# Kernel tuning notes

Hardware: AMD Instinct MI355X
Metric: run time of the kernel (lower is better)

Reference implementation:

```python
import jax, jax.numpy as jnp
import numpy as np

B, N_FEAT, SEQ, E, H, V = 32, 196, 64, 1024, 1024, 32000


def setup_inputs() -> dict:
    key = jax.random.key(0)
    ks = jax.random.split(key, 16)
    s = 0.02
    return {
        "features": jax.random.normal(ks[0], (B, N_FEAT, E), jnp.float32),
        "captions": jax.random.randint(ks[1], (B, SEQ), 0, V),
        "max_seq_length": SEQ,
        # decoder embedding table (vocab, embed)
        "emb": jax.random.normal(ks[2], (V, E), jnp.float32) * s,
        # attention MLP: Linear(E->H), Tanh, Linear(H->1)
        "Wa1": jax.random.normal(ks[3], (H, E), jnp.float32) * s,
        "ba1": jnp.zeros((H,), jnp.float32),
        "Wa2": jax.random.normal(ks[4], (1, H), jnp.float32) * s,
        "ba2": jnp.zeros((1,), jnp.float32),
        # GRU (1 layer), input = concat(word_emb, context) -> E + H
        "W_ih": jax.random.normal(ks[5], (3 * H, E + H), jnp.float32) * s,
        "W_hh": jax.random.normal(ks[6], (3 * H, H), jnp.float32) * s,
        "b_ih": jnp.zeros((3 * H,), jnp.float32),
        "b_hh": jnp.zeros((3 * H,), jnp.float32),
        # output projection Linear(H -> V)
        "W_fc": jax.random.normal(ks[7], (V, H), jnp.float32) * s,
        "b_fc": jnp.zeros((V,), jnp.float32),
    }


def reference(features, captions, max_seq_length, emb, Wa1, ba1, Wa2, ba2,
              W_ih, W_hh, b_ih, b_hh, W_fc, b_fc):
    # words: (B, S, E)
    words = emb[captions]
    # combined: (B, N_FEAT + S, E)
    combined = jnp.concatenate([features, words], axis=1)
    # attention scores over the combined tokens, softmax along token axis
    scores = jnp.tanh(combined @ Wa1.T + ba1) @ Wa2.T + ba2   # (B, M, 1)
    A = jax.nn.softmax(scores, axis=1)                         # (B, M, 1)
    # context h0 = A^T @ combined -> (B, E); used both as GRU h0 and per-step context
    h0 = jnp.sum(A * combined, axis=1)
    context = h0

    def gru_cell(x, h):
        gi = x @ W_ih.T + b_ih          # (B, 3H)
        gh = h @ W_hh.T + b_hh          # (B, 3H)
        ir, iz, inn = jnp.split(gi, 3, axis=-1)
        hr, hz, hn = jnp.split(gh, 3, axis=-1)
        r = jax.nn.sigmoid(ir + hr)
        z = jax.nn.sigmoid(iz + hz)
        n = jnp.tanh(inn + r * hn)
        return (1.0 - z) * n + z * h

    def step(carry, _):
        input_word, h = carry
        x = jnp.concatenate([emb[input_word], context], axis=-1)  # (B, E+H)
        h_new = gru_cell(x, h)
        out = h_new @ W_fc.T + b_fc                               # (B, V)
        # greedy feedback (eval path / no teacher forcing)
        next_word = jnp.argmax(out, axis=-1)
        return (next_word, h_new), out

    init = (captions[:, 0], h0)
    (_, _), outs = jax.lax.scan(step, init, None, length=max_seq_length - 1)
    outs = jnp.transpose(outs, (1, 0, 2))                         # (B, S-1, V)
    bsz = captions.shape[0]
    vocab = W_fc.shape[0]
    outputs = jnp.concatenate(
        [jnp.zeros((bsz, 1, vocab), outs.dtype), outs], axis=1)   # t=0 stays zero
    return outputs, A
```

## Files before the change

### kernel.cpp

```cpp
#include <hip/hip_runtime.h>
#include <hip/hip_bf16.h>

typedef unsigned long long ull;
typedef unsigned int uint;

#define NB 32
#define NFEAT 196
#define SEQL 64
#define ED 1024
#define HD 1024
#define VOC 32000
#define NCOMB 260
#define NROWS (NB*NCOMB)
#define NTILE 2000

typedef __attribute__((ext_vector_type(8))) short s16x8;
typedef __attribute__((ext_vector_type(4))) float f32x4;
typedef __attribute__((ext_vector_type(4))) uint  u32x4;

union FragU { u32x4 u; s16x8 s; };

#define DOT4(acc, wv, xv) acc = fmaf((wv).x,(xv).x, fmaf((wv).y,(xv).y, fmaf((wv).z,(xv).z, fmaf((wv).w,(xv).w,(acc)))))

__device__ __forceinline__ uint enc_f32(float f) {
    uint u = __float_as_uint(f);
    return (u & 0x80000000u) ? ~u : (u | 0x80000000u);
}
__device__ __forceinline__ ull shflxor64(ull v, int m) {
    uint lo = __shfl_xor((uint)v, m);
    uint hi = __shfl_xor((uint)(v >> 32), m);
    return (((ull)hi) << 32) | (ull)lo;
}

__device__ __forceinline__ void split2(float a, float b, uint& hi, uint& lo) {
    __hip_bfloat162 h2 = __float22bfloat162_rn(make_float2(a, b));
    float2 hf = __bfloat1622float2(h2);
    __hip_bfloat162 l2 = __float22bfloat162_rn(make_float2(a - hf.x, b - hf.y));
    hi = *(uint*)&h2;
    lo = *(uint*)&l2;
}

__device__ __forceinline__ void nt_store4(float* p, float a, float b, float c, float d) {
    f32x4 v = {a, b, c, d};
    __builtin_nontemporal_store(v, (f32x4*)p);
}

__global__ void __launch_bounds__(256) k_build(
    const float* __restrict__ features, const int* __restrict__ captions,
    const float* __restrict__ emb, float* __restrict__ combined,
    float* __restrict__ out)
{
    const int bid = blockIdx.x;
    const int t = threadIdx.x;
    if (bid < NROWS) {
        const int b = bid / NCOMB;
        const int i = bid - b*NCOMB;
        const float* src = (i < NFEAT)
            ? (features + ((size_t)(b*NFEAT + i))*ED)
            : (emb + (size_t)captions[b*SEQL + (i - NFEAT)]*ED);
        float4* dst4 = (float4*)(combined + (size_t)bid*ED);
        const float4* s4 = (const float4*)src;
        dst4[t] = s4[t];
    } else {
        const int z = bid - NROWS;
        const int m = z*1024 + t*4;
        if (m < NB*VOC) {
            const int b = m / VOC;
            const int v = m - b*VOC;
            nt_store4(out + (size_t)b*((size_t)SEQL*VOC) + v, 0.f, 0.f, 0.f, 0.f);
        }
    }
}

__global__ void __launch_bounds__(256) k_pack_w1(
    const float* __restrict__ Wa1, uint* __restrict__ W1hi, uint* __restrict__ W1lo)
{
    const int eid = blockIdx.x*256 + threadIdx.x;
    const int lane = eid & 63;
    const int ks = (eid >> 6) & 31;
    const int ct = eid >> 11;
    const int c = ct*16 + (lane & 15);
    const int k0 = ks*32 + ((lane >> 4) & 3)*4;
    const float4 wa = *(const float4*)&Wa1[(size_t)c*ED + k0];
    const float4 wb = *(const float4*)&Wa1[(size_t)c*ED + k0 + 16];
    uint hi[4], lo[4];
    split2(wa.x, wa.y, hi[0], lo[0]);
    split2(wa.z, wa.w, hi[1], lo[1]);
    split2(wb.x, wb.y, hi[2], lo[2]);
    split2(wb.z, wb.w, hi[3], lo[3]);
    *(u32x4*)&W1hi[(size_t)eid*4] = (u32x4){hi[0], hi[1], hi[2], hi[3]};
    *(u32x4*)&W1lo[(size_t)eid*4] = (u32x4){lo[0], lo[1], lo[2], lo[3]};
}

__global__ void __launch_bounds__(256) k_pack_wfc(
    const float* __restrict__ W_fc, uint* __restrict__ Whi, uint* __restrict__ Wlo)
{
    const int eid = blockIdx.x*256 + threadIdx.x;
    const int lane = eid & 63;
    const int ks = (eid >> 6) & 31;
    const int tile = eid >> 11;
    const int row = tile*16 + (lane & 15);
    const int k0 = ks*32 + ((lane >> 4) & 3)*4;
    const float4 wa = *(const float4*)&W_fc[(size_t)row*HD + k0];
    const float4 wb = *(const float4*)&W_fc[(size_t)row*HD + k0 + 16];
    uint hi[4], lo[4];
    split2(wa.x, wa.y, hi[0], lo[0]);
    split2(wa.z, wa.w, hi[1], lo[1]);
    split2(wb.x, wb.y, hi[2], lo[2]);
    split2(wb.z, wb.w, hi[3], lo[3]);
    *(u32x4*)&Whi[(size_t)eid*4] = (u32x4){hi[0], hi[1], hi[2], hi[3]};
    *(u32x4*)&Wlo[(size_t)eid*4] = (u32x4){lo[0], lo[1], lo[2], lo[3]};
}

__global__ void __launch_bounds__(256) k_attn_mfma(
    const float* __restrict__ combined, const uint* __restrict__ W1hi,
    const uint* __restrict__ W1lo, const float* __restrict__ ba1,
    const float* __restrict__ Wa2, float* __restrict__ partials)
{
    const int t = threadIdx.x;
    const int w = t >> 6, l = t & 63;
    const int lane16 = l & 15, qk = (l >> 4) & 3;
    const int rt = blockIdx.x*4 + w;
    const int cg0 = blockIdx.y*2;

    const float* Arow = combined + (size_t)(rt*16 + lane16)*ED;
    const u32x4* bh_base = (const u32x4*)W1hi + l;
    const u32x4* bl_base = (const u32x4*)W1lo + l;

    f32x4 acc[2][4];
#pragma unroll
    for (int c = 0; c < 2; ++c)
#pragma unroll
        for (int i = 0; i < 4; ++i) acc[c][i] = (f32x4){0.f,0.f,0.f,0.f};

#pragma unroll 2
    for (int ks = 0; ks < 32; ++ks) {
        const int k0 = ks*32 + qk*4;
        const float4 aa = *(const float4*)(Arow + k0);
        const float4 ab = *(const float4*)(Arow + k0 + 16);
        FragU ahi, alo;
        uint h0,l0_,h1,l1_,h2,l2_,h3,l3_;
        split2(aa.x, aa.y, h0, l0_);
        split2(aa.z, aa.w, h1, l1_);
        split2(ab.x, ab.y, h2, l2_);
        split2(ab.z, ab.w, h3, l3_);
        ahi.u = (u32x4){h0, h1, h2, h3};
        alo.u = (u32x4){l0_, l1_, l2_, l3_};
#pragma unroll
        for (int c = 0; c < 2; ++c) {
#pragma unroll
            for (int i = 0; i < 4; ++i) {
                const size_t idx = (((size_t)((cg0 + c)*4 + i))*32 + ks)*64;
                FragU bh_, bl_;
                bh_.u = bh_base[idx];
                bl_.u = bl_base[idx];
                acc[c][i] = __builtin_amdgcn_mfma_f32_16x16x32_bf16(ahi.s, bh_.s, acc[c][i], 0, 0, 0);
                acc[c][i] = __builtin_amdgcn_mfma_f32_16x16x32_bf16(ahi.s, bl_.s, acc[c][i], 0, 0, 0);
                acc[c][i] = __builtin_amdgcn_mfma_f32_16x16x32_bf16(alo.s, bh_.s, acc[c][i], 0, 0, 0);
            }
        }
    }

#pragma unroll
    for (int c = 0; c < 2; ++c) {
        const int cg = cg0 + c;
        float s[4];
#pragma unroll
        for (int r = 0; r < 4; ++r) {
            float sum = 0.f;
#pragma unroll
            for (int i = 0; i < 4; ++i) {
                const int col = cg*64 + i*16 + lane16;
                sum += tanhf(acc[c][i][r] + ba1[col]) * Wa2[col];
            }
            s[r] = sum;
        }
#pragma unroll
        for (int m = 1; m <= 8; m <<= 1)
#pragma unroll
            for (int r = 0; r < 4; ++r) s[r] += __shfl_xor(s[r], m);
        if (lane16 == 0) {
#pragma unroll
            for (int r = 0; r < 4; ++r)
                partials[(size_t)(rt*16 + qk*4 + r)*16 + cg] = s[r];
        }
    }
}

__global__ void __launch_bounds__(256) k_attn_finish(
    const float* __restrict__ partials, const float* __restrict__ combined,
    const int* __restrict__ captions,
    float* __restrict__ A_out, float* __restrict__ h0,
    float* __restrict__ ctx, ull* __restrict__ slots0)
{
    const int b = blockIdx.x, t = threadIdx.x;
    __shared__ float sc[NCOMB];
    __shared__ float red[256];

    for (int i = t; i < NCOMB; i += 256) {
        float s = 0.f;
        const float* pr = partials + (size_t)(b*NCOMB + i)*16;
#pragma unroll
        for (int g = 0; g < 16; ++g) s += pr[g];
        sc[i] = s;
    }
    __syncthreads();
    float m = -1e30f;
    for (int i = t; i < NCOMB; i += 256) m = fmaxf(m, sc[i]);
    red[t] = m; __syncthreads();
    for (int s2 = 128; s2 > 0; s2 >>= 1) {
        if (t < s2) red[t] = fmaxf(red[t], red[t+s2]);
        __syncthreads();
    }
    m = red[0]; __syncthreads();
    float ssum = 0.f;
    for (int i = t; i < NCOMB; i += 256) { float e = expf(sc[i] - m); sc[i] = e; ssum += e; }
    red[t] = ssum; __syncthreads();
    for (int s2 = 128; s2 > 0; s2 >>= 1) {
        if (t < s2) red[t] += red[t+s2];
        __syncthreads();
    }
    const float S = red[0]; __syncthreads();
    for (int i = t; i < NCOMB; i += 256) {
        const float a = sc[i] / S;
        sc[i] = a;
        A_out[b*NCOMB + i] = a;
    }
    __syncthreads();
    for (int e = t; e < HD; e += 256) {
        float acc = 0.f;
        const float* cb = combined + (size_t)b*NCOMB*ED + e;
        for (int i = 0; i < NCOMB; ++i) acc = fmaf(sc[i], cb[(size_t)i*ED], acc);
        h0[(size_t)b*HD + e] = acc;
        ctx[(size_t)b*HD + e] = acc;
    }
    if (t == 0) {
        slots0[0*NB + b] = (ull)(~(uint)captions[b*SEQL]);
#pragma unroll
        for (int g = 1; g < 8; ++g) slots0[g*NB + b] = 0ull;
    }
}

__global__ void __launch_bounds__(256) k_gictx(
    const float* __restrict__ W_ih, const float* __restrict__ b_ih,
    const float* __restrict__ ctx, float* __restrict__ gictx)
{
    const int jj = blockIdx.x;
    const int t = threadIdx.x;
    const int w = t >> 6, l = t & 63;
    const int b0 = w*8;
    const float* Wrow = W_ih + (size_t)jj*(ED+HD) + ED;

    float a[8];
#pragma unroll
    for (int i = 0; i < 8; ++i) a[i] = 0.f;
#pragma unroll
    for (int q = 0; q < 4; ++q) {
        const int k = q*256 + l*4;
        const float4 wv = *(const float4*)(Wrow + k);
#pragma unroll
        for (int i = 0; i < 8; ++i) {
            const float4 xv = *(const float4*)(ctx + (size_t)(b0 + i)*HD + k);
            DOT4(a[i], wv, xv);
        }
    }
    int s = (l >> 5) & 1;
    int ib = s*4;
    float tA[4];
#pragma unroll
    for (int ii = 0; ii < 4; ++ii) {
        const float send = a[(1^s)*4 + ii];
        tA[ii] = a[s*4 + ii] + __shfl_xor(send, 32);
    }
    s = (l >> 4) & 1; ib += s*2;
    float tB[2];
#pragma unroll
    for (int jj2 = 0; jj2 < 2; ++jj2) {
        const float send = tA[(1^s)*2 + jj2];
        tB[jj2] = tA[s*2 + jj2] + __shfl_xor(send, 16);
    }
    s = (l >> 3) & 1; ib += s;
    float fg;
    {
        const float send = tB[1^s];
        fg = tB[s] + __shfl_xor(send, 8);
    }
#pragma unroll
    for (int mm = 4; mm >= 1; mm >>= 1) fg += __shfl_xor(fg, mm);
    if ((l & 7) == 0)
        gictx[(size_t)jj*NB + (b0 + ib)] = fg + b_ih[jj];
}

__global__ void __launch_bounds__(256) k_gru(
    const float* __restrict__ emb, const float* __restrict__ W_ih,
    const float* __restrict__ W_hh, const float* __restrict__ gictx,
    const float* __restrict__ b_hh,
    const float* __restrict__ h_prev, float* __restrict__ h_next,
    const ull* __restrict__ slots_prev, ull* __restrict__ slots_cur,
    uint* __restrict__ Hhi, uint* __restrict__ Hlo)
{
    __shared__ int word_s[NB];
    const int t = threadIdx.x;
    if (t < NB) {
        ull best = 0ull;
#pragma unroll
        for (int g = 0; g < 8; ++g) {
            ull k = slots_prev[g*NB + t];
            best = (k > best) ? k : best;
        }
        word_s[t] = (int)(~(uint)best);
    }
    if (blockIdx.x == 0) slots_cur[t] = 0ull;
    __syncthreads();

    const int j = blockIdx.x;
    const int w = t >> 6, l = t & 63;
    const int b0 = w*8;

    float a[4][8];
#pragma unroll
    for (int g = 0; g < 4; ++g)
#pragma unroll
        for (int i = 0; i < 8; ++i) a[g][i] = 0.f;

    const float* Wr = W_ih + (size_t)j*(ED+HD);
    const float* Wz = W_ih + (size_t)(HD + j)*(ED+HD);
    const float* Wn = W_ih + (size_t)(2*HD + j)*(ED+HD);
#pragma unroll
    for (int q = 0; q < 4; ++q) {
        const int k = q*256 + l*4;
        const float4 wr = *(const float4*)(Wr + k);
        const float4 wz = *(const float4*)(Wz + k);
        const float4 wn = *(const float4*)(Wn + k);
#pragma unroll
        for (int i = 0; i < 8; ++i) {
            const float4 xv = *(const float4*)(emb + (size_t)word_s[b0+i]*ED + k);
            DOT4(a[0][i], wr, xv);
            DOT4(a[1][i], wz, xv);
            DOT4(a[2][i], wn, xv);
        }
    }
    const float* Ur = W_hh + (size_t)j*HD;
    const float* Uz = W_hh + (size_t)(HD + j)*HD;
    const float* Un = W_hh + (size_t)(2*HD + j)*HD;
#pragma unroll
    for (int q = 0; q < 4; ++q) {
        const int k = q*256 + l*4;
        const float4 ur = *(const float4*)(Ur + k);
        const float4 uz = *(const float4*)(Uz + k);
        const float4 un = *(const float4*)(Un + k);
#pragma unroll
        for (int i = 0; i < 8; ++i) {
            const float4 hv = *(const float4*)(h_prev + (size_t)(b0+i)*HD + k);
            DOT4(a[0][i], ur, hv);
            DOT4(a[1][i], uz, hv);
            DOT4(a[3][i], un, hv);
        }
    }
    int s = (l >> 5) & 1;
    int ib = s*4;
    float tA[4][4];
#pragma unroll
    for (int g = 0; g < 4; ++g)
#pragma unroll
        for (int ii = 0; ii < 4; ++ii) {
            const float send = a[g][(1^s)*4 + ii];
            tA[g][ii] = a[g][s*4 + ii] + __shfl_xor(send, 32);
        }
    s = (l >> 4) & 1; ib += s*2;
    float tB[4][2];
#pragma unroll
    for (int g = 0; g < 4; ++g)
#pragma unroll
        for (int jj = 0; jj < 2; ++jj) {
            const float send = tA[g][(1^s)*2 + jj];
            tB[g][jj] = tA[g][s*2 + jj] + __shfl_xor(send, 16);
        }
    s = (l >> 3) & 1; ib += s;
    float fg[4];
#pragma unroll
    for (int g = 0; g < 4; ++g) {
        const float send = tB[g][1^s];
        fg[g] = tB[g][s] + __shfl_xor(send, 8);
    }
#pragma unroll
    for (int mm = 4; mm >= 1; mm >>= 1)
#pragma unroll
        for (int g = 0; g < 4; ++g) fg[g] += __shfl_xor(fg[g], mm);

    if ((l & 7) == 0) {
        const int b = b0 + ib;
        const float gcr = gictx[(size_t)j*NB + b];
        const float gcz = gictx[(size_t)(HD + j)*NB + b];
        const float gcn = gictx[(size_t)(2*HD + j)*NB + b];
        const float rg = 1.f/(1.f + expf(-(fg[0] + gcr + b_hh[j])));
        const float zg = 1.f/(1.f + expf(-(fg[1] + gcz + b_hh[HD+j])));
        const float ng = tanhf(fg[2] + gcn + rg*(fg[3] + b_hh[2*HD+j]));
        const float hp = h_prev[(size_t)b*HD + j];
        const float hv = (1.f - zg)*ng + zg*hp;
        h_next[(size_t)b*HD + j] = hv;
        __hip_bfloat16 hb = __float2bfloat16(hv);
        const float hf = __bfloat162float(hb);
        __hip_bfloat16 lb = __float2bfloat16(hv - hf);
        const int bh = b >> 4;
        const int ks = j >> 5;
        const int qk2 = (j >> 2) & 3;
        const int elem = (j & 3) + 4*((j >> 4) & 1);
        const size_t ei = (((size_t)(bh*32 + ks))*64 + qk2*16 + (b & 15))*8 + elem;
        ((ushort*)Hhi)[ei] = *(const ushort*)&hb;
        ((ushort*)Hlo)[ei] = *(const ushort*)&lb;
    }
}

__global__ void __launch_bounds__(256) k_logits(
    const float* __restrict__ W_fc, const uint* __restrict__ Wfchi,
    const uint* __restrict__ Wfclo, const uint* __restrict__ Hhi,
    const uint* __restrict__ Hlo, const float* __restrict__ b_fc,
    float* __restrict__ out, ull* __restrict__ slots_cur, int tstep, int packed)
{
    __shared__ float sm[32][68];
    const int t = threadIdx.x;
    const int w = t >> 6, l = t & 63;
    const int lane16 = l & 15, qk = (l >> 4) & 3;
    const int tile = blockIdx.x*4 + w;

    const u32x4* hh0 = (const u32x4*)Hhi + l;
    const u32x4* hl0 = (const u32x4*)Hlo + l;
    const u32x4* hh1 = (const u32x4*)Hhi + 2048 + l;
    const u32x4* hl1 = (const u32x4*)Hlo + 2048 + l;

    f32x4 acc0 = {0.f,0.f,0.f,0.f};
    f32x4 acc1 = {0.f,0.f,0.f,0.f};

    if (packed) {
        const u32x4* WH = (const u32x4*)Wfchi + (size_t)tile*32*64 + l;
        const u32x4* WL = (const u32x4*)Wfclo + (size_t)tile*32*64 + l;
#pragma unroll 4
        for (int ks = 0; ks < 32; ++ks) {
            FragU whi, wlo, b0h, b0l, b1h, b1l;
            whi.u = WH[ks*64];
            wlo.u = WL[ks*64];
            b0h.u = hh0[ks*64];
            b0l.u = hl0[ks*64];
            b1h.u = hh1[ks*64];
            b1l.u = hl1[ks*64];
            acc0 = __builtin_amdgcn_mfma_f32_16x16x32_bf16(whi.s, b0h.s, acc0, 0, 0, 0);
            acc0 = __builtin_amdgcn_mfma_f32_16x16x32_bf16(whi.s, b0l.s, acc0, 0, 0, 0);
            acc0 = __builtin_amdgcn_mfma_f32_16x16x32_bf16(wlo.s, b0h.s, acc0, 0, 0, 0);
            acc1 = __builtin_amdgcn_mfma_f32_16x16x32_bf16(whi.s, b1h.s, acc1, 0, 0, 0);
            acc1 = __builtin_amdgcn_mfma_f32_16x16x32_bf16(whi.s, b1l.s, acc1, 0, 0, 0);
            acc1 = __builtin_amdgcn_mfma_f32_16x16x32_bf16(wlo.s, b1h.s, acc1, 0, 0, 0);
        }
    } else {
        const float* Wrow = W_fc + (size_t)(tile*16 + lane16)*HD;
#pragma unroll 2
        for (int ks = 0; ks < 32; ++ks) {
            const int k0 = ks*32 + qk*4;
            const float4 wa = *(const float4*)(Wrow + k0);
            const float4 wb = *(const float4*)(Wrow + k0 + 16);
            FragU whi, wlo;
            uint h0,l0_,h1,l1_,h2,l2_,h3,l3_;
            split2(wa.x, wa.y, h0, l0_);
            split2(wa.z, wa.w, h1, l1_);
            split2(wb.x, wb.y, h2, l2_);
            split2(wb.z, wb.w, h3, l3_);
            whi.u = (u32x4){h0, h1, h2, h3};
            wlo.u = (u32x4){l0_, l1_, l2_, l3_};
            FragU b0h, b0l, b1h, b1l;
            b0h.u = hh0[ks*64];
            b0l.u = hl0[ks*64];
            b1h.u = hh1[ks*64];
            b1l.u = hl1[ks*64];
            acc0 = __builtin_amdgcn_mfma_f32_16x16x32_bf16(whi.s, b0h.s, acc0, 0, 0, 0);
            acc0 = __builtin_amdgcn_mfma_f32_16x16x32_bf16(whi.s, b0l.s, acc0, 0, 0, 0);
            acc0 = __builtin_amdgcn_mfma_f32_16x16x32_bf16(wlo.s, b0h.s, acc0, 0, 0, 0);
            acc1 = __builtin_amdgcn_mfma_f32_16x16x32_bf16(whi.s, b1h.s, acc1, 0, 0, 0);
            acc1 = __builtin_amdgcn_mfma_f32_16x16x32_bf16(whi.s, b1l.s, acc1, 0, 0, 0);
            acc1 = __builtin_amdgcn_mfma_f32_16x16x32_bf16(wlo.s, b1h.s, acc1, 0, 0, 0);
        }
    }

    {
        const int rbase = w*16 + qk*4;
        const float4 bias = *(const float4*)&b_fc[blockIdx.x*64 + rbase];
        *(float4*)&sm[lane16][rbase] = make_float4(
            acc0[0] + bias.x, acc0[1] + bias.y, acc0[2] + bias.z, acc0[3] + bias.w);
        *(float4*)&sm[16 + lane16][rbase] = make_float4(
            acc1[0] + bias.x, acc1[1] + bias.y, acc1[2] + bias.z, acc1[3] + bias.w);
    }
    __syncthreads();
    {
        const int b = t >> 3;
        const int rl0 = (t & 7)*8;
        const int vbase = blockIdx.x*64 + rl0;
        float v[8];
        ull bk = 0ull;
#pragma unroll
        for (int e = 0; e < 8; ++e) {
            v[e] = sm[b][rl0 + e];
            const ull key = (((ull)enc_f32(v[e])) << 32) | (ull)(~(uint)(vbase + e));
            bk = (key > bk) ? key : bk;
        }
        float* dst = out + (size_t)b*((size_t)SEQL*VOC) + (size_t)tstep*VOC + vbase;
        nt_store4(dst,     v[0], v[1], v[2], v[3]);
        nt_store4(dst + 4, v[4], v[5], v[6], v[7]);
#pragma unroll
        for (int mm = 4; mm >= 1; mm >>= 1) {
            const ull o = shflxor64(bk, mm);
            bk = (o > bk) ? o : bk;
        }
        if ((t & 7) == 0) atomicMax(slots_cur + (blockIdx.x & 7)*NB + b, bk);
    }
}

extern "C" void kernel_launch(void* const* d_in, const int* in_sizes, int n_in,
                              void* d_out, int out_size, void* d_ws, size_t ws_size,
                              hipStream_t stream)
{
    const float* features = (const float*)d_in[0];
    const int*   captions = (const int*)d_in[1];
    const float* emb  = (const float*)d_in[3];
    const float* Wa1  = (const float*)d_in[4];
    const float* ba1  = (const float*)d_in[5];
    const float* Wa2  = (const float*)d_in[6];
    const float* W_ih = (const float*)d_in[8];
    const float* W_hh = (const float*)d_in[9];
    const float* b_ih = (const float*)d_in[10];
    const float* b_hh = (const float*)d_in[11];
    const float* W_fc = (const float*)d_in[12];
    const float* b_fc = (const float*)d_in[13];

    float* out = (float*)d_out;
    float* A_out = out + (size_t)NB*SEQL*VOC;

    char* wsp = (char*)d_ws;
    float* combined = (float*)wsp;  wsp += (size_t)NROWS*ED*4;
    float* partials = (float*)wsp;  wsp += (size_t)NROWS*16*4;
    float* hbuf0    = (float*)wsp;  wsp += (size_t)NB*HD*4;
    float* hbuf1    = (float*)wsp;  wsp += (size_t)NB*HD*4;
    float* ctx      = (float*)wsp;  wsp += (size_t)NB*HD*4;
    ull*   slots    = (ull*)wsp;    wsp += 2*8*NB*sizeof(ull);
    uint*  Hhi      = (uint*)wsp;   wsp += (size_t)4096*16;
    uint*  Hlo      = (uint*)wsp;   wsp += (size_t)4096*16;
    uint*  W1hi     = (uint*)wsp;   wsp += (size_t)131072*16;
    uint*  W1lo     = (uint*)wsp;   wsp += (size_t)131072*16;
    float* gictx    = (float*)wsp;  wsp += (size_t)3*HD*NB*4;
    uint*  Wfchi    = (uint*)wsp;   wsp += (size_t)NTILE*32*64*16;
    uint*  Wfclo    = (uint*)wsp;   wsp += (size_t)NTILE*32*64*16;
    size_t packed_need = (size_t)(wsp - (char*)d_ws);
    const int packed = (ws_size >= packed_need) ? 1 : 0;

    k_build<<<NROWS + 1000, 256, 0, stream>>>(features, captions, emb, combined, out);
    k_pack_w1<<<512, 256, 0, stream>>>(Wa1, W1hi, W1lo);
    if (packed)
        k_pack_wfc<<<NTILE*32*64/256, 256, 0, stream>>>(W_fc, Wfchi, Wfclo);
    k_attn_mfma<<<dim3(130, 8), 256, 0, stream>>>(combined, W1hi, W1lo, ba1, Wa2, partials);
    k_attn_finish<<<NB, 256, 0, stream>>>(partials, combined, captions,
                                          A_out, hbuf0, ctx, slots);
    k_gictx<<<3*HD, 256, 0, stream>>>(W_ih, b_ih, ctx, gictx);
    for (int t = 1; t < SEQL; ++t) {
        const float* hp = (t & 1) ? hbuf0 : hbuf1;
        float*       hn = (t & 1) ? hbuf1 : hbuf0;
        const ull* sp = slots + (size_t)((t - 1) & 1)*8*NB;
        ull*       scur = slots + (size_t)(t & 1)*8*NB;
        k_gru<<<1024, 256, 0, stream>>>(emb, W_ih, W_hh, gictx, b_hh,
                                        hp, hn, sp, scur, Hhi, Hlo);
        k_logits<<<NTILE/4, 256, 0, stream>>>(W_fc, Wfchi, Wfclo, Hhi, Hlo, b_fc,
                                              out, scur, t, packed);
    }
}
```

Baseline: 3.840 ms.

## Split-K logits waves over two tiles each and widen attention column groups

The logits kernel now has each wave compute two 16-row vocab tiles over half of K (split-K across wave pairs). The two partial sums are merged through shared memory, so each H fragment load is reused for two weight tiles and the per-wave dependent MFMA chain is halved. The attention MFMA kernel now processes four column groups per block instead of two, which halves grid.y and reuses each A-row split across more columns. This raises register pressure, adds an LDS merge and an extra barrier in logits, and lowers attention block count.

```diff
diff --git a/kernel.cpp b/kernel.cpp
--- a/kernel.cpp
+++ b/kernel.cpp
@@ -121,19 +121,18 @@
     const int w = t >> 6, l = t & 63;
     const int lane16 = l & 15, qk = (l >> 4) & 3;
     const int rt = blockIdx.x*4 + w;
-    const int cg0 = blockIdx.y*2;
+    const int cg0 = blockIdx.y*4;
 
     const float* Arow = combined + (size_t)(rt*16 + lane16)*ED;
     const u32x4* bh_base = (const u32x4*)W1hi + l;
     const u32x4* bl_base = (const u32x4*)W1lo + l;
 
-    f32x4 acc[2][4];
-#pragma unroll
-    for (int c = 0; c < 2; ++c)
+    f32x4 acc[4][4];
+#pragma unroll
+    for (int c = 0; c < 4; ++c)
 #pragma unroll
         for (int i = 0; i < 4; ++i) acc[c][i] = (f32x4){0.f,0.f,0.f,0.f};
 
-#pragma unroll 2
     for (int ks = 0; ks < 32; ++ks) {
         const int k0 = ks*32 + qk*4;
         const float4 aa = *(const float4*)(Arow + k0);
@@ -147,7 +146,7 @@
         ahi.u = (u32x4){h0, h1, h2, h3};
         alo.u = (u32x4){l0_, l1_, l2_, l3_};
 #pragma unroll
-        for (int c = 0; c < 2; ++c) {
+        for (int c = 0; c < 4; ++c) {
 #pragma unroll
             for (int i = 0; i < 4; ++i) {
                 const size_t idx = (((size_t)((cg0 + c)*4 + i))*32 + ks)*64;
@@ -162,7 +161,7 @@
     }
 
 #pragma unroll
-    for (int c = 0; c < 2; ++c) {
+    for (int c = 0; c < 4; ++c) {
         const int cg = cg0 + c;
         float s[4];
 #pragma unroll
@@ -419,74 +418,120 @@
     float* __restrict__ out, ull* __restrict__ slots_cur, int tstep, int packed)
 {
     __shared__ float sm[32][68];
+    __shared__ float mergebuf[2][64][16];
     const int t = threadIdx.x;
     const int w = t >> 6, l = t & 63;
     const int lane16 = l & 15, qk = (l >> 4) & 3;
-    const int tile = blockIdx.x*4 + w;
-
-    const u32x4* hh0 = (const u32x4*)Hhi + l;
-    const u32x4* hl0 = (const u32x4*)Hlo + l;
-    const u32x4* hh1 = (const u32x4*)Hhi + 2048 + l;
-    const u32x4* hl1 = (const u32x4*)Hlo + 2048 + l;
-
-    f32x4 acc0 = {0.f,0.f,0.f,0.f};
-    f32x4 acc1 = {0.f,0.f,0.f,0.f};
+    const int tp = w & 1;
+    const int kh = w >> 1;
+    const int tile0 = blockIdx.x*4 + tp*2;
+
+    const u32x4* hh0 = (const u32x4*)Hhi + (size_t)(kh*16)*64 + l;
+    const u32x4* hl0 = (const u32x4*)Hlo + (size_t)(kh*16)*64 + l;
+    const u32x4* hh1 = (const u32x4*)Hhi + (size_t)(32 + kh*16)*64 + l;
+    const u32x4* hl1 = (const u32x4*)Hlo + (size_t)(32 + kh*16)*64 + l;
+
+    f32x4 accA0 = {0.f,0.f,0.f,0.f};
+    f32x4 accA1 = {0.f,0.f,0.f,0.f};
+    f32x4 accB0 = {0.f,0.f,0.f,0.f};
+    f32x4 accB1 = {0.f,0.f,0.f,0.f};
 
     if (packed) {
-        const u32x4* WH = (const u32x4*)Wfchi + (size_t)tile*32*64 + l;
-        const u32x4* WL = (const u32x4*)Wfclo + (size_t)tile*32*64 + l;
-#pragma unroll 4
-        for (int ks = 0; ks < 32; ++ks) {
-            FragU whi, wlo, b0h, b0l, b1h, b1l;
-            whi.u = WH[ks*64];
-            wlo.u = WL[ks*64];
+        const u32x4* WHa = (const u32x4*)Wfchi + ((size_t)tile0*32 + kh*16)*64 + l;
+        const u32x4* WLa = (const u32x4*)Wfclo + ((size_t)tile0*32 + kh*16)*64 + l;
+        const u32x4* WHb = WHa + (size_t)32*64;
+        const u32x4* WLb = WLa + (size_t)32*64;
+#pragma unroll 2
+        for (int ks = 0; ks < 16; ++ks) {
+            FragU wha, wla, whb, wlb, b0h, b0l, b1h, b1l;
+            wha.u = WHa[ks*64];
+            wla.u = WLa[ks*64];
+            whb.u = WHb[ks*64];
+            wlb.u = WLb[ks*64];
             b0h.u = hh0[ks*64];
             b0l.u = hl0[ks*64];
             b1h.u = hh1[ks*64];
             b1l.u = hl1[ks*64];
-            acc0 = __builtin_amdgcn_mfma_f32_16x16x32_bf16(whi.s, b0h.s, acc0, 0, 0, 0);
-            acc0 = __builtin_amdgcn_mfma_f32_16x16x32_bf16(whi.s, b0l.s, acc0, 0, 0, 0);
-            acc0 = __builtin_amdgcn_mfma_f32_16x16x32_bf16(wlo.s, b0h.s, acc0, 0, 0, 0);
-            acc1 = __builtin_amdgcn_mfma_f32_16x16x32_bf16(whi.s, b1h.s, acc1, 0, 0, 0);
-            acc1 = __builtin_amdgcn_mfma_f32_16x16x32_bf16(whi.s, b1l.s, acc1, 0, 0, 0);
-            acc1 = __builtin_amdgcn_mfma_f32_16x16x32_bf16(wlo.s, b1h.s, acc1, 0, 0, 0);
+            accA0 = __builtin_amdgcn_mfma_f32_16x16x32_bf16(wha.s, b0h.s, accA0, 0, 0, 0);
+            accA0 = __builtin_amdgcn_mfma_f32_16x16x32_bf16(wha.s, b0l.s, accA0, 0, 0, 0);
+            accA0 = __builtin_amdgcn_mfma_f32_16x16x32_bf16(wla.s, b0h.s, accA0, 0, 0, 0);
+            accA1 = __builtin_amdgcn_mfma_f32_16x16x32_bf16(wha.s, b1h.s, accA1, 0, 0, 0);
+            accA1 = __builtin_amdgcn_mfma_f32_16x16x32_bf16(wha.s, b1l.s, accA1, 0, 0, 0);
+            accA1 = __builtin_amdgcn_mfma_f32_16x16x32_bf16(wla.s, b1h.s, accA1, 0, 0, 0);
+            accB0 = __builtin_amdgcn_mfma_f32_16x16x32_bf16(whb.s, b0h.s, accB0, 0, 0, 0);
+            accB0 = __builtin_amdgcn_mfma_f32_16x16x32_bf16(whb.s, b0l.s, accB0, 0, 0, 0);
+            accB0 = __builtin_amdgcn_mfma_f32_16x16x32_bf16(wlb.s, b0h.s, accB0, 0, 0, 0);
+            accB1 = __builtin_amdgcn_mfma_f32_16x16x32_bf16(whb.s, b1h.s, accB1, 0, 0, 0);
+            accB1 = __builtin_amdgcn_mfma_f32_16x16x32_bf16(whb.s, b1l.s, accB1, 0, 0, 0);
+            accB1 = __builtin_amdgcn_mfma_f32_16x16x32_bf16(wlb.s, b1h.s, accB1, 0, 0, 0);
         }
     } else {
-        const float* Wrow = W_fc + (size_t)(tile*16 + lane16)*HD;
+        const float* WrowA = W_fc + (size_t)(tile0*16 + lane16)*HD;
+        const float* WrowB = W_fc + (size_t)((tile0 + 1)*16 + lane16)*HD;
 #pragma unroll 2
-        for (int ks = 0; ks < 32; ++ks) {
-            const int k0 = ks*32 + qk*4;
-            const float4 wa = *(const float4*)(Wrow + k0);
-            const float4 wb = *(const float4*)(Wrow + k0 + 16);
-            FragU whi, wlo;
+        for (int ks = 0; ks < 16; ++ks) {
+            const int k0 = (kh*16 + ks)*32 + qk*4;
+            const float4 waA = *(const float4*)(WrowA + k0);
+            const float4 wbA = *(const float4*)(WrowA + k0 + 16);
+            const float4 waB = *(const float4*)(WrowB + k0);
+            const float4 wbB = *(const float4*)(WrowB + k0 + 16);
+            FragU wha, wla, whb, wlb;
             uint h0,l0_,h1,l1_,h2,l2_,h3,l3_;
-            split2(wa.x, wa.y, h0, l0_);
-            split2(wa.z, wa.w, h1, l1_);
-            split2(wb.x, wb.y, h2, l2_);
-            split2(wb.z, wb.w, h3, l3_);
-            whi.u = (u32x4){h0, h1, h2, h3};
-            wlo.u = (u32x4){l0_, l1_, l2_, l3_};
+            split2(waA.x, waA.y, h0, l0_);
+            split2(waA.z, waA.w, h1, l1_);
+            split2(wbA.x, wbA.y, h2, l2_);
+            split2(wbA.z, wbA.w, h3, l3_);
+            wha.u = (u32x4){h0, h1, h2, h3};
+            wla.u = (u32x4){l0_, l1_, l2_, l3_};
+            split2(waB.x, waB.y, h0, l0_);
+            split2(waB.z, waB.w, h1, l1_);
+            split2(wbB.x, wbB.y, h2, l2_);
+            split2(wbB.z, wbB.w, h3, l3_);
+            whb.u = (u32x4){h0, h1, h2, h3};
+            wlb.u = (u32x4){l0_, l1_, l2_, l3_};
             FragU b0h, b0l, b1h, b1l;
             b0h.u = hh0[ks*64];
             b0l.u = hl0[ks*64];
             b1h.u = hh1[ks*64];
             b1l.u = hl1[ks*64];
-            acc0 = __builtin_amdgcn_mfma_f32_16x16x32_bf16(whi.s, b0h.s, acc0, 0, 0, 0);
-            acc0 = __builtin_amdgcn_mfma_f32_16x16x32_bf16(whi.s, b0l.s, acc0, 0, 0, 0);
-            acc0 = __builtin_amdgcn_mfma_f32_16x16x32_bf16(wlo.s, b0h.s, acc0, 0, 0, 0);
-            acc1 = __builtin_amdgcn_mfma_f32_16x16x32_bf16(whi.s, b1h.s, acc1, 0, 0, 0);
-            acc1 = __builtin_amdgcn_mfma_f32_16x16x32_bf16(whi.s, b1l.s, acc1, 0, 0, 0);
-            acc1 = __builtin_amdgcn_mfma_f32_16x16x32_bf16(wlo.s, b1h.s, acc1, 0, 0, 0);
-        }
-    }
-
-    {
-        const int rbase = w*16 + qk*4;
-        const float4 bias = *(const float4*)&b_fc[blockIdx.x*64 + rbase];
-        *(float4*)&sm[lane16][rbase] = make_float4(
-            acc0[0] + bias.x, acc0[1] + bias.y, acc0[2] + bias.z, acc0[3] + bias.w);
-        *(float4*)&sm[16 + lane16][rbase] = make_float4(
-            acc1[0] + bias.x, acc1[1] + bias.y, acc1[2] + bias.z, acc1[3] + bias.w);
+            accA0 = __builtin_amdgcn_mfma_f32_16x16x32_bf16(wha.s, b0h.s, accA0, 0, 0, 0);
+            accA0 = __builtin_amdgcn_mfma_f32_16x16x32_bf16(wha.s, b0l.s, accA0, 0, 0, 0);
+            accA0 = __builtin_amdgcn_mfma_f32_16x16x32_bf16(wla.s, b0h.s, accA0, 0, 0, 0);
+            accA1 = __builtin_amdgcn_mfma_f32_16x16x32_bf16(wha.s, b1h.s, accA1, 0, 0, 0);
+            accA1 = __builtin_amdgcn_mfma_f32_16x16x32_bf16(wha.s, b1l.s, accA1, 0, 0, 0);
+            accA1 = __builtin_amdgcn_mfma_f32_16x16x32_bf16(wla.s, b1h.s, accA1, 0, 0, 0);
+            accB0 = __builtin_amdgcn_mfma_f32_16x16x32_bf16(whb.s, b0h.s, accB0, 0, 0, 0);
+            accB0 = __builtin_amdgcn_mfma_f32_16x16x32_bf16(whb.s, b0l.s, accB0, 0, 0, 0);
+            accB0 = __builtin_amdgcn_mfma_f32_16x16x32_bf16(wlb.s, b0h.s, accB0, 0, 0, 0);
+            accB1 = __builtin_amdgcn_mfma_f32_16x16x32_bf16(whb.s, b1h.s, accB1, 0, 0, 0);
+            accB1 = __builtin_amdgcn_mfma_f32_16x16x32_bf16(whb.s, b1l.s, accB1, 0, 0, 0);
+            accB1 = __builtin_amdgcn_mfma_f32_16x16x32_bf16(wlb.s, b1h.s, accB1, 0, 0, 0);
+        }
+    }
+
+    if (kh == 1) {
+        float* rr = &mergebuf[tp][l][0];
+        *(float4*)&rr[0]  = make_float4(accA0[0], accA0[1], accA0[2], accA0[3]);
+        *(float4*)&rr[4]  = make_float4(accA1[0], accA1[1], accA1[2], accA1[3]);
+        *(float4*)&rr[8]  = make_float4(accB0[0], accB0[1], accB0[2], accB0[3]);
+        *(float4*)&rr[12] = make_float4(accB1[0], accB1[1], accB1[2], accB1[3]);
+    }
+    __syncthreads();
+    if (kh == 0) {
+        const float* rr = &mergebuf[tp][l][0];
+        const float4 biasA = *(const float4*)&b_fc[tile0*16 + qk*4];
+        const float4 biasB = *(const float4*)&b_fc[(tile0 + 1)*16 + qk*4];
+#pragma unroll
+        for (int r = 0; r < 4; ++r) {
+            const int rlocA = tp*32 + qk*4 + r;
+            const int rlocB = tp*32 + 16 + qk*4 + r;
+            const float bA = (&biasA.x)[r];
+            const float bB = (&biasB.x)[r];
+            sm[lane16][rlocA]      = accA0[r] + rr[r]      + bA;
+            sm[16 + lane16][rlocA] = accA1[r] + rr[4 + r]  + bA;
+            sm[lane16][rlocB]      = accB0[r] + rr[8 + r]  + bB;
+            sm[16 + lane16][rlocB] = accB1[r] + rr[12 + r] + bB;
+        }
     }
     __syncthreads();
     {
@@ -554,7 +599,7 @@
     k_pack_w1<<<512, 256, 0, stream>>>(Wa1, W1hi, W1lo);
     if (packed)
         k_pack_wfc<<<NTILE*32*64/256, 256, 0, stream>>>(W_fc, Wfchi, Wfclo);
-    k_attn_mfma<<<dim3(130, 8), 256, 0, stream>>>(combined, W1hi, W1lo, ba1, Wa2, partials);
+    k_attn_mfma<<<dim3(130, 4), 256, 0, stream>>>(combined, W1hi, W1lo, ba1, Wa2, partials);
     k_attn_finish<<<NB, 256, 0, stream>>>(partials, combined, captions,
                                           A_out, hbuf0, ctx, slots);
     k_gictx<<<3*HD, 256, 0, stream>>>(W_ih, b_ih, ctx, gictx);
```

New measurement: 3.821 ms. Within noise of the previous version (-0.5%).
